# Kernel tuning notes

Measured on AMD Instinct MI355X. Metric: run time of the kernel, lower is better.

The kernel has to match this reference:

```python
import jax, jax.numpy as jnp
import numpy as np

B, S, D, H, HD, F = 2, 2048, 1024, 16, 64, 4096
EPS = 1e-5


def layer_norm(x, g, b):
    m = jnp.mean(x, axis=-1, keepdims=True)
    v = jnp.var(x, axis=-1, keepdims=True)
    return (x - m) * jax.lax.rsqrt(v + EPS) * g + b


def setup_inputs() -> dict:
    key = jax.random.key(0)
    ks = jax.random.split(key, 8)
    hidden_states = jax.random.normal(ks[0], (B, S, D), dtype=jnp.float32)
    # additive causal mask: 0 where allowed, -1e9 where masked
    causal = jnp.tril(jnp.ones((S, S), dtype=bool))
    attention_mask = jnp.where(causal, 0.0, -1e9).astype(jnp.float32)[None, None]
    sd = 1.0 / np.sqrt(D)
    Wq = jax.random.normal(ks[1], (D, D), jnp.float32) * sd
    Wk = jax.random.normal(ks[2], (D, D), jnp.float32) * sd
    Wv = jax.random.normal(ks[3], (D, D), jnp.float32) * sd
    Wo = jax.random.normal(ks[4], (D, D), jnp.float32) * sd
    W1 = jax.random.normal(ks[5], (D, F), jnp.float32) * sd
    W2 = jax.random.normal(ks[6], (F, D), jnp.float32) * (1.0 / np.sqrt(F))
    ln1_g = jnp.ones((D,), jnp.float32)
    ln1_b = jnp.zeros((D,), jnp.float32)
    ln2_g = jnp.ones((D,), jnp.float32)
    ln2_b = jnp.zeros((D,), jnp.float32)
    return dict(hidden_states=hidden_states, attention_mask=attention_mask,
                ln1_g=ln1_g, ln1_b=ln1_b, Wq=Wq, Wk=Wk, Wv=Wv, Wo=Wo,
                ln2_g=ln2_g, ln2_b=ln2_b, W1=W1, W2=W2)


def reference(hidden_states, attention_mask, ln1_g, ln1_b, Wq, Wk, Wv, Wo,
              ln2_g, ln2_b, W1, W2):
    x = hidden_states
    # --- attention sublayer (pre-LN) ---
    h = layer_norm(x, ln1_g, ln1_b)
    q = (h @ Wq).reshape(B, S, H, HD).transpose(0, 2, 1, 3)  # b h s d
    k = (h @ Wk).reshape(B, S, H, HD).transpose(0, 2, 1, 3)
    v = (h @ Wv).reshape(B, S, H, HD).transpose(0, 2, 1, 3)
    scores = jnp.einsum('bhqd,bhkd->bhqk', q, k) / np.sqrt(HD)
    scores = scores + attention_mask
    attn = jax.nn.softmax(scores, axis=-1)
    ctx = jnp.einsum('bhqk,bhkd->bhqd', attn, v)
    ctx = ctx.transpose(0, 2, 1, 3).reshape(B, S, D)
    x = x + ctx @ Wo
    # --- FFN sublayer (pre-LN) ---
    h = layer_norm(x, ln2_g, ln2_b)
    h = jax.nn.gelu(h @ W1, approximate=False) @ W2
    out = x + h
    return out, k, v
```

## Files before the change

### kernel.cpp

```cpp
#include <hip/hip_runtime.h>
#include <hip/hip_bf16.h>
#include <cstdint>
#include <cstddef>

#define BB 2
#define SS 2048
#define DD 1024
#define HH 16
#define HDIM 64
#define FF 4096
#define RR (BB*SS)

typedef __attribute__((ext_vector_type(8))) short short8;
typedef __attribute__((ext_vector_type(4))) float floatx4;

__device__ __forceinline__ unsigned short f2bf(float f){
    __hip_bfloat16 h = __float2bfloat16(f);
    return *reinterpret_cast<unsigned short*>(&h);
}

__device__ __forceinline__ void load_lds16(const void* g, void* l){
    __builtin_amdgcn_global_load_lds((__attribute__((address_space(1))) void*)g,
                                     (__attribute__((address_space(3))) void*)l, 16, 0, 0);
}


template<int BN, int EPI, int NBUF = 1>
__global__ __launch_bounds__(256, 3) void gemm_bt(const unsigned short* __restrict__ A,
                                                  const unsigned short* __restrict__ B,
                                                  int M, int N, int K, int KS,
                                                  float* __restrict__ cf,
                                                  const float* __restrict__ resid,
                                                  unsigned short* __restrict__ cbf,
                                                  unsigned short* __restrict__ qb,
                                                  float* __restrict__ kout,
                                                  unsigned short* __restrict__ kbf,
                                                  float* __restrict__ vout)
{
    constexpr int MI_M = (BN==128) ? 4 : 2;
    __shared__ __align__(16) unsigned short As[NBUF][128*64];
    __shared__ __align__(16) unsigned short Bs[NBUF][BN*64];
    const int tid  = threadIdx.x;
    const int lane = tid & 63;
    const int wave = tid >> 6;
    const int quad = lane >> 4, l15 = lane & 15;
    const int wrow = (BN==128) ? (wave>>1)*64 : wave*32;
    const int wcol = (BN==128) ? (wave&1)*64 : 0;

    const unsigned gx = gridDim.x;
    const unsigned nwg = gx * gridDim.y;
    const unsigned bid = blockIdx.y * gx + blockIdx.x;
    const unsigned cpx = nwg >> 3;
    const unsigned swz = (bid & 7) * cpx + (bid >> 3);
    const int bx = (int)(swz % gx), by = (int)(swz / gx);

    const int gm0 = by * 128, gn0 = bx * BN;
    const int k0 = blockIdx.z * KS;
    const int niter = KS >> 6;
    const int phase = (int)((unsigned)(bx + by) % (unsigned)niter);

    floatx4 acc[MI_M][4];
#pragma unroll
    for (int i=0;i<MI_M;i++)
#pragma unroll
        for (int j=0;j<4;j++) acc[i][j] = (floatx4){0.f,0.f,0.f,0.f};

    const int rsub = lane >> 3;
    const int d8   = (lane & 7) * 8;
    const int ksub = ((lane & 7) ^ rsub) * 8;
    constexpr int nchw = (128 + BN) / 32;

    auto stage = [&](int kt, int buf){
#pragma unroll
        for (int i=0;i<nchw;i++){
            int c = wave*nchw + i;
            if (c < 16)
                load_lds16(A + (size_t)(gm0 + c*8 + rsub)*K + kt + ksub,
                           &As[buf][c*512 + rsub*64 + d8]);
            else
                load_lds16(B + (size_t)(gn0 + (c-16)*8 + rsub)*K + kt + ksub,
                           &Bs[buf][(c-16)*512 + rsub*64 + d8]);
        }
    };

    auto compute = [&](const unsigned short* as, const unsigned short* bs){
#pragma unroll
        for (int kk=0; kk<64; kk+=32){
            const int cb4 = kk >> 3;
            short8 af[MI_M], bfr[4];
#pragma unroll
            for (int mi=0;mi<MI_M;mi++){
                int row = wrow + mi*16 + l15;
                af[mi] = *(const short8*)&as[row*64 + (((cb4+quad) ^ (row&7)))*8];
            }
#pragma unroll
            for (int ni=0;ni<4;ni++){
                int row = wcol + ni*16 + l15;
                bfr[ni] = *(const short8*)&bs[row*64 + (((cb4+quad) ^ (row&7)))*8];
            }
#pragma unroll
            for (int mi=0;mi<MI_M;mi++)
#pragma unroll
                for (int ni=0;ni<4;ni++)
                    acc[mi][ni] = __builtin_amdgcn_mfma_f32_16x16x32_bf16(af[mi], bfr[ni], acc[mi][ni], 0, 0, 0);
        }
    };

    if constexpr (NBUF == 1){
        for (int it=0; it<niter; it++){
            int j = it + phase; if (j >= niter) j -= niter;
            stage(k0 + j*64, 0);
            __syncthreads();
            compute(As[0], Bs[0]);
            __syncthreads();
        }
    } else {
        stage(k0 + phase*64, 0);
        int cur = 0;
        for (int it=0; it<niter; it++){
            __syncthreads();
            if (it+1 < niter){
                int j = it + 1 + phase; if (j >= niter) j -= niter;
                stage(k0 + j*64, cur^1);
            }
            compute(As[cur], Bs[cur]);
            cur ^= 1;
        }
    }

#pragma unroll
    for (int mi=0;mi<MI_M;mi++)
#pragma unroll
        for (int ni=0;ni<4;ni++)
#pragma unroll
            for (int r=0;r<4;r++){
                int row = gm0 + wrow + mi*16 + quad*4 + r;
                int col = gn0 + wcol + ni*16 + l15;
                float v = acc[mi][ni][r];
                if constexpr (EPI == 1){
                    int region = gn0 >> 10;
                    if (region == 0){
                        qb[(size_t)row*1024 + col] = f2bf(v);
                    } else {
                        int c1 = col & 1023;
                        int h = c1 >> 6, d = c1 & 63;
                        int b = row >> 11, s = row & (SS-1);
                        size_t o = ((size_t)((b*HH + h)*SS + s))*HDIM + d;
                        if (region == 1){ kout[o] = v; kbf[o] = f2bf(v); }
                        else            { vout[o] = v; }
                    }
                } else if constexpr (EPI == 2){
                    size_t o = (size_t)row*N + col;
                    cf[o] = v + resid[o];
                } else if constexpr (EPI == 3){
                    float u = v*(0.79788456f + 0.0356774081f*v*v);
                    float g = v / (1.f + exp2f(-2.88539008f*u));
                    cbf[(size_t)row*N + col] = f2bf(g);
                } else {
                    cf[(size_t)blockIdx.z*M*N + (size_t)row*N + col] = v;
                }
            }
}

__global__ __launch_bounds__(256) void combine2_kernel(const float* __restrict__ p0,
                                                       const float* __restrict__ p1,
                                                       const float* __restrict__ resid,
                                                       float* __restrict__ out, int n4)
{
    const int i = blockIdx.x*256 + threadIdx.x;
    if (i >= n4) return;
    float4 a = ((const float4*)p0)[i];
    float4 b = ((const float4*)p1)[i];
    float4 c = ((const float4*)resid)[i];
    ((float4*)out)[i] = make_float4(a.x+b.x+c.x, a.y+b.y+c.y, a.z+b.z+c.z, a.w+b.w+c.w);
}

__global__ __launch_bounds__(256) void attn_kernel(const unsigned short* __restrict__ qbf,
                                                   const unsigned short* __restrict__ kbf,
                                                   const unsigned short* __restrict__ vtbf,
                                                   unsigned short* __restrict__ ctx)
{
    __shared__ unsigned short Ks[2][64*64];
    __shared__ unsigned short Vs[2][64*64];
    __shared__ unsigned short Ps[4][16*64];
    const int tid  = threadIdx.x;
    const int lane = tid & 63;
    const int wave = tid >> 6;
    const int quad = lane >> 4, l15 = lane & 15;
    const int aqt = blockIdx.x;
    const int bqt = 31 - aqt;
    const int bh = blockIdx.y;
    const int b = bh >> 4, h = bh & 15;
    const int q0a = aqt * 64, q0b = bqt * 64;

    const unsigned short* kb  = kbf  + (size_t)bh * SS * HDIM;
    const unsigned short* vtb = vtbf + (size_t)bh * HDIM * SS;

    const unsigned short* qra = qbf + (size_t)(b*SS + q0a + wave*16 + l15)*DD + h*HDIM + quad*8;
    const unsigned short* qrb = qbf + (size_t)(b*SS + q0b + wave*16 + l15)*DD + h*HDIM + quad*8;
    short8 qa0 = *(const short8*)qra;
    short8 qa1 = *(const short8*)(qra + 32);
    short8 qb0 = *(const short8*)qrb;
    short8 qb1 = *(const short8*)(qrb + 32);

    float lpA[4] = {0.f,0.f,0.f,0.f}, lpB[4] = {0.f,0.f,0.f,0.f};
    floatx4 accA[4], accB[4];
#pragma unroll
    for (int n=0;n<4;n++){ accA[n] = (floatx4){0.f,0.f,0.f,0.f}; accB[n] = (floatx4){0.f,0.f,0.f,0.f}; }

    const int r8 = lane >> 3;
    const int c8 = ((lane & 7) ^ r8) * 8;
    const int d8 = (lane & 7) * 8;
    const int nkt = bqt + 1;
    const float SC = 0.125f * 1.44269504f;

#pragma unroll
    for (int p=0;p<2;p++){
        int row = p*32 + wave*8 + r8;
        load_lds16(kb  + (size_t)row*HDIM + c8,  &Ks[0][row*64 + d8]);
        load_lds16(vtb + (size_t)row*SS   + c8,  &Vs[0][row*64 + d8]);
    }

    unsigned short* pl = Ps[wave];
    int cur = 0;
    for (int kt=0; kt<nkt; kt++){
        __syncthreads();
        if (kt+1 < nkt){
            int nb = cur ^ 1;
#pragma unroll
            for (int p=0;p<2;p++){
                int row = p*32 + wave*8 + r8;
                load_lds16(kb  + (size_t)((kt+1)*64 + row)*HDIM + c8, &Ks[nb][row*64 + d8]);
                load_lds16(vtb + (size_t)row*SS + (size_t)(kt+1)*64 + c8, &Vs[nb][row*64 + d8]);
            }
        }
        const unsigned short* ks = Ks[cur];
        const unsigned short* vs = Vs[cur];

        short8 kf0[4], kf1[4];
#pragma unroll
        for (int j=0;j<4;j++){
            int row = j*16 + l15;
            kf0[j] = *(const short8*)&ks[row*64 + ((quad     ^ (row&7)))*8];
            kf1[j] = *(const short8*)&ks[row*64 + (((quad+4) ^ (row&7)))*8];
        }
        short8 vf0[4], vf1[4];
#pragma unroll
        for (int n=0;n<4;n++){
            int row = n*16 + l15;
            vf0[n] = *(const short8*)&vs[row*64 + ((quad     ^ (row&7)))*8];
            vf1[n] = *(const short8*)&vs[row*64 + (((quad+4) ^ (row&7)))*8];
        }

        {
            floatx4 s[4];
#pragma unroll
            for (int j=0;j<4;j++){
                floatx4 zz = (floatx4){0.f,0.f,0.f,0.f};
                zz = __builtin_amdgcn_mfma_f32_16x16x32_bf16(qb0, kf0[j], zz, 0, 0, 0);
                zz = __builtin_amdgcn_mfma_f32_16x16x32_bf16(qb1, kf1[j], zz, 0, 0, 0);
                s[j] = zz;
            }
#pragma unroll
            for (int j=0;j<4;j++)
#pragma unroll
                for (int r=0;r<4;r++){
                    int prow = quad*4 + r;
                    float p = exp2f(s[j][r]*SC);
                    if (kt == bqt){
                        int row = q0b + wave*16 + prow;
                        int col = kt*64 + j*16 + l15;
                        if (col > row) p = 0.f;
                    }
                    lpB[r] += p;
                    int ch = (2*j + (l15>>3)) ^ (prow&7);
                    pl[prow*64 + ch*8 + (l15&7)] = f2bf(p);
                }
            short8 pf0 = *(const short8*)&pl[l15*64 + ((quad     ^ (l15&7)))*8];
            short8 pf1 = *(const short8*)&pl[l15*64 + (((quad+4) ^ (l15&7)))*8];
#pragma unroll
            for (int n=0;n<4;n++){
                accB[n] = __builtin_amdgcn_mfma_f32_16x16x32_bf16(pf0, vf0[n], accB[n], 0, 0, 0);
                accB[n] = __builtin_amdgcn_mfma_f32_16x16x32_bf16(pf1, vf1[n], accB[n], 0, 0, 0);
            }
        }

        if (kt <= aqt){
            floatx4 s[4];
#pragma unroll
            for (int j=0;j<4;j++){
                floatx4 zz = (floatx4){0.f,0.f,0.f,0.f};
                zz = __builtin_amdgcn_mfma_f32_16x16x32_bf16(qa0, kf0[j], zz, 0, 0, 0);
                zz = __builtin_amdgcn_mfma_f32_16x16x32_bf16(qa1, kf1[j], zz, 0, 0, 0);
                s[j] = zz;
            }
#pragma unroll
            for (int j=0;j<4;j++)
#pragma unroll
                for (int r=0;r<4;r++){
                    int prow = quad*4 + r;
                    float p = exp2f(s[j][r]*SC);
                    if (kt == aqt){
                        int row = q0a + wave*16 + prow;
                        int col = kt*64 + j*16 + l15;
                        if (col > row) p = 0.f;
                    }
                    lpA[r] += p;
                    int ch = (2*j + (l15>>3)) ^ (prow&7);
                    pl[prow*64 + ch*8 + (l15&7)] = f2bf(p);
                }
            short8 pf0 = *(const short8*)&pl[l15*64 + ((quad     ^ (l15&7)))*8];
            short8 pf1 = *(const short8*)&pl[l15*64 + (((quad+4) ^ (l15&7)))*8];
#pragma unroll
            for (int n=0;n<4;n++){
                accA[n] = __builtin_amdgcn_mfma_f32_16x16x32_bf16(pf0, vf0[n], accA[n], 0, 0, 0);
                accA[n] = __builtin_amdgcn_mfma_f32_16x16x32_bf16(pf1, vf1[n], accA[n], 0, 0, 0);
            }
        }
        cur ^= 1;
    }

#pragma unroll
    for (int r=0;r<4;r++){
        float va = lpA[r], vb = lpB[r];
        va += __shfl_xor(va, 1); vb += __shfl_xor(vb, 1);
        va += __shfl_xor(va, 2); vb += __shfl_xor(vb, 2);
        va += __shfl_xor(va, 4); vb += __shfl_xor(vb, 4);
        va += __shfl_xor(va, 8); vb += __shfl_xor(vb, 8);
        lpA[r] = va; lpB[r] = vb;
    }
#pragma unroll
    for (int n=0;n<4;n++)
#pragma unroll
        for (int r=0;r<4;r++){
            float oa = accA[n][r] / lpA[r];
            float ob = accB[n][r] / lpB[r];
            ctx[(size_t)(b*SS + q0a + wave*16 + quad*4 + r)*DD + h*HDIM + n*16 + l15] = f2bf(oa);
            ctx[(size_t)(b*SS + q0b + wave*16 + quad*4 + r)*DD + h*HDIM + n*16 + l15] = f2bf(ob);
        }
}

__global__ __launch_bounds__(256) void ln_kernel(const float* __restrict__ x,
                                                 const float* __restrict__ g,
                                                 const float* __restrict__ bparm,
                                                 unsigned short* __restrict__ out)
{
    __shared__ float red[8];
    const int row = blockIdx.x;
    const int tid = threadIdx.x;
    const float* xr = x + (size_t)row*DD;
    float4 v = *(const float4*)(xr + tid*4);
    float s  = v.x+v.y+v.z+v.w;
    float sq = v.x*v.x + v.y*v.y + v.z*v.z + v.w*v.w;
#pragma unroll
    for (int off=1; off<64; off<<=1){ s += __shfl_xor(s, off); sq += __shfl_xor(sq, off); }
    if ((tid & 63) == 0){ red[tid>>6] = s; red[4 + (tid>>6)] = sq; }
    __syncthreads();
    float ts = red[0]+red[1]+red[2]+red[3];
    float tq = red[4]+red[5]+red[6]+red[7];
    float mean = ts * (1.f/DD);
    float var  = tq * (1.f/DD) - mean*mean;
    float inv  = rsqrtf(var + 1e-5f);
    float4 gv = *(const float4*)(g + tid*4);
    float4 bv = *(const float4*)(bparm + tid*4);
    ushort4 o;
    o.x = f2bf((v.x-mean)*inv*gv.x + bv.x);
    o.y = f2bf((v.y-mean)*inv*gv.y + bv.y);
    o.z = f2bf((v.z-mean)*inv*gv.z + bv.z);
    o.w = f2bf((v.w-mean)*inv*gv.w + bv.w);
    *(ushort4*)(out + (size_t)row*DD + tid*4) = o;
}

__global__ __launch_bounds__(256) void castT_kernel(const float* __restrict__ in,
                                                    unsigned short* __restrict__ out,
                                                    int R, int C)
{
    __shared__ float t[32][33];
    const size_t zoff = (size_t)blockIdx.z * R * C;
    in  += zoff; out += zoff;
    const int tr = blockIdx.y*32, tc = blockIdx.x*32;
    const int lr = threadIdx.x >> 5, lc = threadIdx.x & 31;
#pragma unroll
    for (int i=0;i<4;i++)
        t[lr + i*8][lc] = in[(size_t)(tr + lr + i*8)*C + tc + lc];
    __syncthreads();
#pragma unroll
    for (int i=0;i<4;i++)
        out[(size_t)(tc + lr + i*8)*R + tr + lc] = f2bf(t[lc][lr + i*8]);
}

__global__ __launch_bounds__(256) void castT4_kernel(const float* __restrict__ i0,
                                                     const float* __restrict__ i1,
                                                     const float* __restrict__ i2,
                                                     const float* __restrict__ i3,
                                                     unsigned short* __restrict__ o0,
                                                     unsigned short* __restrict__ o1,
                                                     unsigned short* __restrict__ o2,
                                                     unsigned short* __restrict__ o3)
{
    __shared__ float t[32][33];
    const int z = blockIdx.z;
    const float* in = (z==0) ? i0 : (z==1) ? i1 : (z==2) ? i2 : i3;
    unsigned short* out = (z==0) ? o0 : (z==1) ? o1 : (z==2) ? o2 : o3;
    const int tr = blockIdx.y*32, tc = blockIdx.x*32;
    const int lr = threadIdx.x >> 5, lc = threadIdx.x & 31;
#pragma unroll
    for (int i=0;i<4;i++)
        t[lr + i*8][lc] = in[(size_t)(tr + lr + i*8)*1024 + tc + lc];
    __syncthreads();
#pragma unroll
    for (int i=0;i<4;i++)
        out[(size_t)(tc + lr + i*8)*1024 + tr + lc] = f2bf(t[lc][lr + i*8]);
}

extern "C" void kernel_launch(void* const* d_in, const int* in_sizes, int n_in,
                              void* d_out, int out_size, void* d_ws, size_t ws_size,
                              hipStream_t stream)
{
    const float* x     = (const float*)d_in[0];
    const float* ln1_g = (const float*)d_in[2];
    const float* ln1_b = (const float*)d_in[3];
    const float* Wq    = (const float*)d_in[4];
    const float* Wk    = (const float*)d_in[5];
    const float* Wv    = (const float*)d_in[6];
    const float* Wo    = (const float*)d_in[7];
    const float* ln2_g = (const float*)d_in[8];
    const float* ln2_b = (const float*)d_in[9];
    const float* W1    = (const float*)d_in[10];
    const float* W2    = (const float*)d_in[11];

    float* out  = (float*)d_out;
    float* kout = out  + (size_t)RR*DD;
    float* vout = kout + (size_t)BB*HH*SS*HDIM;

    char* w = (char*)d_ws;
    auto alloc = [&](size_t bytes) -> char* {
        char* p = w; w += (bytes + 255) & ~(size_t)255; return p;
    };
    unsigned short* qkvT  = (unsigned short*)alloc((size_t)3072*1024*2);
    unsigned short* WoT   = (unsigned short*)alloc((size_t)1024*1024*2);
    unsigned short* W1T   = (unsigned short*)alloc((size_t)4096*1024*2);
    unsigned short* W2T   = (unsigned short*)alloc((size_t)1024*4096*2);
    unsigned short* h_bf  = (unsigned short*)alloc((size_t)RR*DD*2);
    unsigned short* q_bf  = (unsigned short*)alloc((size_t)RR*DD*2);
    unsigned short* k_bf  = (unsigned short*)alloc((size_t)RR*DD*2);
    unsigned short* vt_bf = (unsigned short*)alloc((size_t)RR*DD*2);
    unsigned short* ctx_bf= (unsigned short*)alloc((size_t)RR*DD*2);
    unsigned short* act_bf= (unsigned short*)alloc((size_t)RR*FF*2);
    float* x1     = (float*)alloc((size_t)RR*DD*4);
    float* fpart  = (float*)alloc((size_t)2*RR*DD*4);

    castT4_kernel<<<dim3(32,32,4), 256, 0, stream>>>(
        Wq, Wk, Wv, Wo, qkvT, qkvT + 1024*1024, qkvT + 2*1024*1024, WoT);
    castT_kernel<<<dim3(128,32,1), 256, 0, stream>>>(W1, W1T, 1024, 4096);
    castT_kernel<<<dim3(32,128,1), 256, 0, stream>>>(W2, W2T, 4096, 1024);

    ln_kernel<<<RR, 256, 0, stream>>>(x, ln1_g, ln1_b, h_bf);
    gemm_bt<128,1,1><<<dim3(3072/128, RR/128), 256, 0, stream>>>(
        h_bf, qkvT, RR, 3072, 1024, 1024, nullptr, nullptr, nullptr, q_bf, kout, k_bf, vout);
    castT_kernel<<<dim3(2, 64, BB*HH), 256, 0, stream>>>(vout, vt_bf, SS, HDIM);
    attn_kernel<<<dim3(16, BB*HH), 256, 0, stream>>>(q_bf, k_bf, vt_bf, ctx_bf);
    gemm_bt<64,2,1><<<dim3(1024/64, RR/128), 256, 0, stream>>>(
        ctx_bf, WoT, RR, 1024, 1024, 1024, x1, x, nullptr, nullptr, nullptr, nullptr, nullptr);

    ln_kernel<<<RR, 256, 0, stream>>>(x1, ln2_g, ln2_b, h_bf);
    gemm_bt<128,3,1><<<dim3(4096/128, RR/128), 256, 0, stream>>>(
        h_bf, W1T, RR, 4096, 1024, 1024, nullptr, nullptr, act_bf, nullptr, nullptr, nullptr, nullptr);
    gemm_bt<128,4,1><<<dim3(1024/128, RR/128, 2), 256, 0, stream>>>(
        act_bf, W2T, RR, 1024, 4096, 2048, fpart, nullptr, nullptr, nullptr, nullptr, nullptr, nullptr);
    combine2_kernel<<<(RR*DD/4 + 255)/256, 256, 0, stream>>>(
        fpart, fpart + (size_t)RR*DD, x1, out, RR*DD/4);
}
```

Baseline: 365.1 us.

## Split attention KV loop and interleave both query tiles with separate P buffers

Splits the causal attention key loop into a phase where both paired query tiles are active and a tail where only the longer tile runs. The per-iteration `kt <= aqt` branch and the B-tile mask check leave the first phase. Each wave gets separate LDS P buffers for the two tiles, so the QK MFMAs, softmax exps and PV MFMAs of A and B can be interleaved for more instruction-level parallelism. In exchange it raises register pressure by holding both score sets live, doubles P scratch LDS, and duplicates code.

```diff
diff --git a/kernel.cpp b/kernel.cpp
--- a/kernel.cpp
+++ b/kernel.cpp
@@ -182,7 +182,7 @@
 {
     __shared__ unsigned short Ks[2][64*64];
     __shared__ unsigned short Vs[2][64*64];
-    __shared__ unsigned short Ps[4][16*64];
+    __shared__ unsigned short Ps[4][2][16*64];
     const int tid  = threadIdx.x;
     const int lane = tid & 63;
     const int wave = tid >> 6;
@@ -214,16 +214,23 @@
     const int nkt = bqt + 1;
     const float SC = 0.125f * 1.44269504f;
 
-#pragma unroll
-    for (int p=0;p<2;p++){
-        int row = p*32 + wave*8 + r8;
-        load_lds16(kb  + (size_t)row*HDIM + c8,  &Ks[0][row*64 + d8]);
-        load_lds16(vtb + (size_t)row*SS   + c8,  &Vs[0][row*64 + d8]);
-    }
-
-    unsigned short* pl = Ps[wave];
+    auto stageKV = [&](int kt, int buf){
+#pragma unroll
+        for (int p=0;p<2;p++){
+            int row = p*32 + wave*8 + r8;
+            load_lds16(kb  + (size_t)(kt*64 + row)*HDIM + c8, &Ks[buf][row*64 + d8]);
+            load_lds16(vtb + (size_t)row*SS + (size_t)kt*64 + c8, &Vs[buf][row*64 + d8]);
+        }
+    };
+
+    stageKV(0, 0);
+
+    unsigned short* plB = Ps[wave][0];
+    unsigned short* plA = Ps[wave][1];
     int cur = 0;
-    for (int kt=0; kt<nkt; kt++){
+    int kt = 0;
+
+    for (; kt <= aqt; kt++){
         __syncthreads();
         if (kt+1 < nkt){
             int nb = cur ^ 1;
@@ -252,70 +259,125 @@
             vf1[n] = *(const short8*)&vs[row*64 + (((quad+4) ^ (row&7)))*8];
         }
 
-        {
-            floatx4 s[4];
-#pragma unroll
-            for (int j=0;j<4;j++){
-                floatx4 zz = (floatx4){0.f,0.f,0.f,0.f};
-                zz = __builtin_amdgcn_mfma_f32_16x16x32_bf16(qb0, kf0[j], zz, 0, 0, 0);
-                zz = __builtin_amdgcn_mfma_f32_16x16x32_bf16(qb1, kf1[j], zz, 0, 0, 0);
-                s[j] = zz;
-            }
-#pragma unroll
-            for (int j=0;j<4;j++)
-#pragma unroll
-                for (int r=0;r<4;r++){
-                    int prow = quad*4 + r;
-                    float p = exp2f(s[j][r]*SC);
-                    if (kt == bqt){
-                        int row = q0b + wave*16 + prow;
-                        int col = kt*64 + j*16 + l15;
-                        if (col > row) p = 0.f;
-                    }
-                    lpB[r] += p;
-                    int ch = (2*j + (l15>>3)) ^ (prow&7);
-                    pl[prow*64 + ch*8 + (l15&7)] = f2bf(p);
+        floatx4 sB[4], sA[4];
+#pragma unroll
+        for (int j=0;j<4;j++){
+            floatx4 zz = (floatx4){0.f,0.f,0.f,0.f};
+            zz = __builtin_amdgcn_mfma_f32_16x16x32_bf16(qb0, kf0[j], zz, 0, 0, 0);
+            zz = __builtin_amdgcn_mfma_f32_16x16x32_bf16(qb1, kf1[j], zz, 0, 0, 0);
+            sB[j] = zz;
+        }
+#pragma unroll
+        for (int j=0;j<4;j++){
+            floatx4 zz = (floatx4){0.f,0.f,0.f,0.f};
+            zz = __builtin_amdgcn_mfma_f32_16x16x32_bf16(qa0, kf0[j], zz, 0, 0, 0);
+            zz = __builtin_amdgcn_mfma_f32_16x16x32_bf16(qa1, kf1[j], zz, 0, 0, 0);
+            sA[j] = zz;
+        }
+
+#pragma unroll
+        for (int j=0;j<4;j++)
+#pragma unroll
+            for (int r=0;r<4;r++){
+                int prow = quad*4 + r;
+                float p = exp2f(sB[j][r]*SC);
+                lpB[r] += p;
+                int ch = (2*j + (l15>>3)) ^ (prow&7);
+                plB[prow*64 + ch*8 + (l15&7)] = f2bf(p);
+            }
+        short8 pfB0 = *(const short8*)&plB[l15*64 + ((quad     ^ (l15&7)))*8];
+        short8 pfB1 = *(const short8*)&plB[l15*64 + (((quad+4) ^ (l15&7)))*8];
+
+#pragma unroll
+        for (int j=0;j<4;j++)
+#pragma unroll
+            for (int r=0;r<4;r++){
+                int prow = quad*4 + r;
+                float p = exp2f(sA[j][r]*SC);
+                if (kt == aqt){
+                    int row = q0a + wave*16 + prow;
+                    int col = kt*64 + j*16 + l15;
+                    if (col > row) p = 0.f;
                 }
-            short8 pf0 = *(const short8*)&pl[l15*64 + ((quad     ^ (l15&7)))*8];
-            short8 pf1 = *(const short8*)&pl[l15*64 + (((quad+4) ^ (l15&7)))*8];
-#pragma unroll
-            for (int n=0;n<4;n++){
-                accB[n] = __builtin_amdgcn_mfma_f32_16x16x32_bf16(pf0, vf0[n], accB[n], 0, 0, 0);
-                accB[n] = __builtin_amdgcn_mfma_f32_16x16x32_bf16(pf1, vf1[n], accB[n], 0, 0, 0);
-            }
-        }
-
-        if (kt <= aqt){
-            floatx4 s[4];
-#pragma unroll
-            for (int j=0;j<4;j++){
-                floatx4 zz = (floatx4){0.f,0.f,0.f,0.f};
-                zz = __builtin_amdgcn_mfma_f32_16x16x32_bf16(qa0, kf0[j], zz, 0, 0, 0);
-                zz = __builtin_amdgcn_mfma_f32_16x16x32_bf16(qa1, kf1[j], zz, 0, 0, 0);
-                s[j] = zz;
-            }
-#pragma unroll
-            for (int j=0;j<4;j++)
-#pragma unroll
-                for (int r=0;r<4;r++){
-                    int prow = quad*4 + r;
-                    float p = exp2f(s[j][r]*SC);
-                    if (kt == aqt){
-                        int row = q0a + wave*16 + prow;
-                        int col = kt*64 + j*16 + l15;
-                        if (col > row) p = 0.f;
-                    }
-                    lpA[r] += p;
-                    int ch = (2*j + (l15>>3)) ^ (prow&7);
-                    pl[prow*64 + ch*8 + (l15&7)] = f2bf(p);
+                lpA[r] += p;
+                int ch = (2*j + (l15>>3)) ^ (prow&7);
+                plA[prow*64 + ch*8 + (l15&7)] = f2bf(p);
+            }
+
+#pragma unroll
+        for (int n=0;n<4;n++){
+            accB[n] = __builtin_amdgcn_mfma_f32_16x16x32_bf16(pfB0, vf0[n], accB[n], 0, 0, 0);
+            accB[n] = __builtin_amdgcn_mfma_f32_16x16x32_bf16(pfB1, vf1[n], accB[n], 0, 0, 0);
+        }
+
+        short8 pfA0 = *(const short8*)&plA[l15*64 + ((quad     ^ (l15&7)))*8];
+        short8 pfA1 = *(const short8*)&plA[l15*64 + (((quad+4) ^ (l15&7)))*8];
+#pragma unroll
+        for (int n=0;n<4;n++){
+            accA[n] = __builtin_amdgcn_mfma_f32_16x16x32_bf16(pfA0, vf0[n], accA[n], 0, 0, 0);
+            accA[n] = __builtin_amdgcn_mfma_f32_16x16x32_bf16(pfA1, vf1[n], accA[n], 0, 0, 0);
+        }
+        cur ^= 1;
+    }
+
+    for (; kt < nkt; kt++){
+        __syncthreads();
+        if (kt+1 < nkt){
+            int nb = cur ^ 1;
+#pragma unroll
+            for (int p=0;p<2;p++){
+                int row = p*32 + wave*8 + r8;
+                load_lds16(kb  + (size_t)((kt+1)*64 + row)*HDIM + c8, &Ks[nb][row*64 + d8]);
+                load_lds16(vtb + (size_t)row*SS + (size_t)(kt+1)*64 + c8, &Vs[nb][row*64 + d8]);
+            }
+        }
+        const unsigned short* ks = Ks[cur];
+        const unsigned short* vs = Vs[cur];
+
+        short8 kf0[4], kf1[4];
+#pragma unroll
+        for (int j=0;j<4;j++){
+            int row = j*16 + l15;
+            kf0[j] = *(const short8*)&ks[row*64 + ((quad     ^ (row&7)))*8];
+            kf1[j] = *(const short8*)&ks[row*64 + (((quad+4) ^ (row&7)))*8];
+        }
+        short8 vf0[4], vf1[4];
+#pragma unroll
+        for (int n=0;n<4;n++){
+            int row = n*16 + l15;
+            vf0[n] = *(const short8*)&vs[row*64 + ((quad     ^ (row&7)))*8];
+            vf1[n] = *(const short8*)&vs[row*64 + (((quad+4) ^ (row&7)))*8];
+        }
+
+        floatx4 sB[4];
+#pragma unroll
+        for (int j=0;j<4;j++){
+            floatx4 zz = (floatx4){0.f,0.f,0.f,0.f};
+            zz = __builtin_amdgcn_mfma_f32_16x16x32_bf16(qb0, kf0[j], zz, 0, 0, 0);
+            zz = __builtin_amdgcn_mfma_f32_16x16x32_bf16(qb1, kf1[j], zz, 0, 0, 0);
+            sB[j] = zz;
+        }
+#pragma unroll
+        for (int j=0;j<4;j++)
+#pragma unroll
+            for (int r=0;r<4;r++){
+                int prow = quad*4 + r;
+                float p = exp2f(sB[j][r]*SC);
+                if (kt == bqt){
+                    int row = q0b + wave*16 + prow;
+                    int col = kt*64 + j*16 + l15;
+                    if (col > row) p = 0.f;
                 }
-            short8 pf0 = *(const short8*)&pl[l15*64 + ((quad     ^ (l15&7)))*8];
-            short8 pf1 = *(const short8*)&pl[l15*64 + (((quad+4) ^ (l15&7)))*8];
-#pragma unroll
-            for (int n=0;n<4;n++){
-                accA[n] = __builtin_amdgcn_mfma_f32_16x16x32_bf16(pf0, vf0[n], accA[n], 0, 0, 0);
-                accA[n] = __builtin_amdgcn_mfma_f32_16x16x32_bf16(pf1, vf1[n], accA[n], 0, 0, 0);
-            }
+                lpB[r] += p;
+                int ch = (2*j + (l15>>3)) ^ (prow&7);
+                plB[prow*64 + ch*8 + (l15&7)] = f2bf(p);
+            }
+        short8 pfB0 = *(const short8*)&plB[l15*64 + ((quad     ^ (l15&7)))*8];
+        short8 pfB1 = *(const short8*)&plB[l15*64 + (((quad+4) ^ (l15&7)))*8];
+#pragma unroll
+        for (int n=0;n<4;n++){
+            accB[n] = __builtin_amdgcn_mfma_f32_16x16x32_bf16(pfB0, vf0[n], accB[n], 0, 0, 0);
+            accB[n] = __builtin_amdgcn_mfma_f32_16x16x32_bf16(pfB1, vf1[n], accB[n], 0, 0, 0);
         }
         cur ^= 1;
     }
```

After: 375.7 us. 1.03x slower.
